# Optimization experiments

Hardware: AMD Instinct MI355X
Metric: run time of the kernel (lower is better)

The kernel has to match this reference:

```python
import jax, jax.numpy as jnp
import numpy as np

N_T = 100  # number of time grid points for the ODE solve, matching torch.linspace(0, 1, 100)


def setup_inputs() -> dict:
    key = jax.random.key(0)
    kx, kw, kb, kc, kd = jax.random.split(key, 5)
    H = 1024
    N = 16384
    return {
        "x": jax.random.normal(kx, (N, H), dtype=jnp.float32),
        "W": jax.random.normal(kw, (H, H), dtype=jnp.float32),
        "b": jax.random.normal(kb, (H,), dtype=jnp.float32),
        "c": jax.random.normal(kc, (H,), dtype=jnp.float32),
        "d": jax.random.normal(kd, (H,), dtype=jnp.float32),
    }


def reference(x, W, b, c, d):
    # fused matmul + trig elementwise: z = x @ W + b*sin(x) + c*cos(x) + d*tan(x)
    z = jnp.matmul(x, W) + b * jnp.sin(x) + c * jnp.cos(x) + d * jnp.tan(x)

    # ODE: dy/dt = -y + t*z, y(0)=0, integrated on linspace(0,1,100), return y(1).
    ts = jnp.linspace(0.0, 1.0, N_T, dtype=z.dtype)
    t0 = ts[:-1]
    dts = ts[1:] - ts[:-1]

    def f(t, y):
        return -y + t * z

    def rk4_step(y, t_dt):
        t, dt = t_dt
        k1 = f(t, y)
        k2 = f(t + 0.5 * dt, y + 0.5 * dt * k1)
        k3 = f(t + 0.5 * dt, y + 0.5 * dt * k2)
        k4 = f(t + dt, y + dt * k3)
        y_next = y + (dt / 6.0) * (k1 + 2.0 * k2 + 2.0 * k3 + k4)
        return y_next, None

    y0 = jnp.zeros_like(z)
    y_final, _ = jax.lax.scan(rk4_step, y0, (t0, dts))
    return y_final
```

## Files before the change

### kernel.cpp

```cpp
#include <hip/hip_runtime.h>
#include <hip/hip_bf16.h>

typedef __attribute__((ext_vector_type(4))) float  f32x4;
typedef __attribute__((ext_vector_type(8))) short  bf16x8;
typedef __attribute__((ext_vector_type(4))) short  bf16x4v;

#define EPAD 68
#define AS1 __attribute__((address_space(1)))
#define AS3 __attribute__((address_space(3)))

__device__ __forceinline__ unsigned short f2bf(float f) {
  __hip_bfloat16 h = __float2bfloat16(f);
  unsigned short u; __builtin_memcpy(&u, &h, 2); return u;
}
__device__ __forceinline__ float bf2f(short u) {
  unsigned int w = ((unsigned int)(unsigned short)u) << 16;
  float f; __builtin_memcpy(&f, &w, 4); return f;
}

__device__ __forceinline__ void my_sincos(float xf, float& s_out, float& c_out) {
  const float kf = __builtin_rintf(xf * 0.636619772367581343f);
  const int   q  = (int)kf;
  const double kd = (double)kf;
  double rd = __builtin_fma(-kd, 1.5707963267948966,    (double)xf);
  rd        = __builtin_fma(-kd, 6.123233995736766e-17, rd);
  const float r = (float)rd;
  const float z = r * r;
  const float ps = fmaf(z, fmaf(z, fmaf(z, 2.7183114939898219e-06f,
                                           -1.9839334836096632e-04f),
                                   8.3333293858894632e-03f),
                        -1.6666666641626524e-01f);
  const float sr = fmaf(r * z, ps, r);
  const float pc = fmaf(z, fmaf(z, fmaf(z, 2.4390448796277409e-05f,
                                           -1.3886763774609929e-03f),
                                   4.1666623323739063e-02f),
                        -4.9999999725103100e-01f);
  const float cr = fmaf(z, pc, 1.0f);
  const bool swap = (q & 1) != 0;
  float s1 = swap ? cr : sr;
  float c1 = swap ? sr : cr;
  if (q & 2)       s1 = -s1;
  if ((q + 1) & 2) c1 = -c1;
  s_out = s1; c_out = c1;
}

__global__ __launch_bounds__(256)
void prep_all(const float* __restrict__ W, const float* __restrict__ x,
              const float* __restrict__ bv, const float* __restrict__ cv,
              const float* __restrict__ dv,
              unsigned short* __restrict__ Wt, unsigned short* __restrict__ xb,
              unsigned short* __restrict__ g, int H, int n4) {
  __shared__ float tile[64][65];
  const int t = threadIdx.x;
  if (blockIdx.x < 256) {
    const int blk = blockIdx.x;
    const int n0 = (blk & 15) << 6;
    const int k0 = (blk >> 4) << 6;
    #pragma unroll
    for (int it = 0; it < 4; ++it) {
      int q = it * 256 + t;
      int r = q >> 4, c4 = (q & 15) << 2;
      f32x4 v = *(const f32x4*)&W[(size_t)(k0 + r) * H + n0 + c4];
      tile[r][c4 + 0] = v[0]; tile[r][c4 + 1] = v[1];
      tile[r][c4 + 2] = v[2]; tile[r][c4 + 3] = v[3];
    }
    __syncthreads();
    #pragma unroll
    for (int it = 0; it < 4; ++it) {
      int q = it * 256 + t;
      int r = q >> 4, c4 = (q & 15) << 2;
      bf16x4v o;
      #pragma unroll
      for (int j = 0; j < 4; ++j) o[j] = (short)f2bf(tile[c4 + j][r]);
      *(bf16x4v*)&Wt[(size_t)(n0 + r) * H + k0 + c4] = o;
    }
  } else {
    const int jm = (H >> 2) - 1;
    int i = (blockIdx.x - 256) * 256 + t;
    const int stride = ((int)gridDim.x - 256) * 256;
    for (; i < n4; i += stride) {
      f32x4 v = ((const f32x4*)x)[i];
      const int j4 = (i & jm) << 2;
      f32x4 b4 = *(const f32x4*)&bv[j4];
      f32x4 c4 = *(const f32x4*)&cv[j4];
      f32x4 d4 = *(const f32x4*)&dv[j4];
      bf16x4v xo, go;
      #pragma unroll
      for (int e = 0; e < 4; ++e) {
        xo[e] = (short)f2bf(v[e]);
        float s, co;
        my_sincos(v[e], s, co);
        const float tn = s * __builtin_amdgcn_rcpf(co);
        go[e] = (short)f2bf(fmaf(b4[e], s, fmaf(c4[e], co, d4[e] * tn)));
      }
      ((bf16x4v*)xb)[i] = xo;
      ((bf16x4v*)g)[i]  = go;
    }
  }
}

__global__ __launch_bounds__(256)
void transpose_W(const float* __restrict__ W, unsigned short* __restrict__ Wt, int H) {
  __shared__ float tile[64][65];
  const int k0 = blockIdx.y * 64;
  const int n0 = blockIdx.x * 64;
  const int t = threadIdx.x;
  #pragma unroll
  for (int it = 0; it < 4; ++it) {
    int q = it * 256 + t;
    int r = q >> 4, c4 = (q & 15) << 2;
    f32x4 v = *(const f32x4*)&W[(size_t)(k0 + r) * H + n0 + c4];
    tile[r][c4 + 0] = v[0]; tile[r][c4 + 1] = v[1];
    tile[r][c4 + 2] = v[2]; tile[r][c4 + 3] = v[3];
  }
  __syncthreads();
  #pragma unroll
  for (int it = 0; it < 4; ++it) {
    int q = it * 256 + t;
    int r = q >> 4, c4 = (q & 15) << 2;
    bf16x4v o;
    #pragma unroll
    for (int j = 0; j < 4; ++j) o[j] = (short)f2bf(tile[c4 + j][r]);
    *(bf16x4v*)&Wt[(size_t)(n0 + r) * H + k0 + c4] = o;
  }
}
__global__ __launch_bounds__(256)
void cvt_x(const float* __restrict__ x, unsigned short* __restrict__ xb, int n4) {
  int i = blockIdx.x * 256 + threadIdx.x;
  const int stride = gridDim.x * 256;
  for (; i < n4; i += stride) {
    f32x4 v = ((const f32x4*)x)[i];
    bf16x4v o;
    #pragma unroll
    for (int j = 0; j < 4; ++j) o[j] = (short)f2bf(v[j]);
    ((bf16x4v*)xb)[i] = o;
  }
}

__global__ __launch_bounds__(512, 2)
void gemm_256(const unsigned short* __restrict__ xb,
              const unsigned short* __restrict__ Wt,
              const unsigned short* __restrict__ g,
              float* __restrict__ out, float S, int H) {
  __shared__ unsigned char smem[98304];
  float* Es = (float*)smem;

  const int tid  = threadIdx.x;
  const int nwg  = gridDim.x;
  const int work = (blockIdx.x & 7) * (nwg >> 3) + (blockIdx.x >> 3);
  const int nbj  = H >> 8;
  const int bj   = work % nbj;
  const int bi   = work / nbj;
  const int i0   = bi * 256, j0 = bj * 256;
  const int wave = tid >> 6, lane = tid & 63;
  const int wr   = wave >> 2, wc = wave & 3;
  const int l16  = lane & 15, lq = lane >> 4;

  const unsigned short *aS0, *aS1, *bS0, *bS1;
  {
    const int D0 = tid * 16,        sup0 = D0 >> 7;
    const int sl0 = ((D0 >> 4) & 7) ^ (sup0 & 7);
    const int r0  = sup0 * 2 + (sl0 >> 2), c0 = (sl0 & 3) << 3;
    const int D1 = 8192 + tid * 16, sup1 = D1 >> 7;
    const int sl1 = ((D1 >> 4) & 7) ^ (sup1 & 7);
    const int r1  = sup1 * 2 + (sl1 >> 2), c1 = (sl1 & 3) << 3;
    aS0 = &xb[(size_t)(i0 + r0) * H + c0];
    aS1 = &xb[(size_t)(i0 + r1) * H + c1];
    bS0 = &Wt[(size_t)(j0 + r0) * H + c0];
    bS1 = &Wt[(size_t)(j0 + r1) * H + c1];
  }

  #define STAGE(bufq, kOff)                                                     \
    do {                                                                        \
      char* _b = (char*)smem + (bufq) * 32768;                                  \
      __builtin_amdgcn_global_load_lds((const AS1 void*)(aS0 + (kOff)),         \
        (AS3 void*)(_b + tid * 16), 16, 0, 0);                                  \
      __builtin_amdgcn_global_load_lds((const AS1 void*)(aS1 + (kOff)),         \
        (AS3 void*)(_b + 8192 + tid * 16), 16, 0, 0);                           \
      __builtin_amdgcn_global_load_lds((const AS1 void*)(bS0 + (kOff)),         \
        (AS3 void*)(_b + 16384 + tid * 16), 16, 0, 0);                          \
      __builtin_amdgcn_global_load_lds((const AS1 void*)(bS1 + (kOff)),         \
        (AS3 void*)(_b + 24576 + tid * 16), 16, 0, 0);                          \
    } while (0)

  const int slot  = (4 * (l16 & 1) + lq) ^ ((l16 >> 1) & 7);
  const int laneT = (l16 >> 1) * 128 + slot * 16;
  const int aBase = wr * 8192 + laneT;
  const int bBase = wc * 4096 + laneT;

  f32x4 acc[8][4] = {};

  const int nsteps = H >> 5;
  STAGE(0, 0);
  STAGE(1, 32);
  int bufc = 0;
  for (int t = 0; t < nsteps; ++t) {
    if (t + 2 < nsteps) {
      int buf2 = bufc + 2; if (buf2 >= 3) buf2 -= 3;
      STAGE(buf2, (t + 2) * 32);
      asm volatile("s_waitcnt vmcnt(8)" ::: "memory");
    } else if (t + 2 == nsteps) {
      asm volatile("s_waitcnt vmcnt(4)" ::: "memory");
    } else {
      asm volatile("s_waitcnt vmcnt(0)" ::: "memory");
    }
    __builtin_amdgcn_s_barrier();
    asm volatile("" ::: "memory");
    const char* Ab = (const char*)smem + bufc * 32768;
    const char* Bb = Ab + 16384;
    bf16x8 bfr[4];
    #pragma unroll
    for (int ni = 0; ni < 4; ++ni)
      bfr[ni] = *(const bf16x8*)(Bb + bBase + ni * 1024);
    __builtin_amdgcn_s_setprio(1);
    #pragma unroll
    for (int mi = 0; mi < 8; ++mi) {
      bf16x8 af = *(const bf16x8*)(Ab + aBase + mi * 1024);
      #pragma unroll
      for (int ni = 0; ni < 4; ++ni)
        acc[mi][ni] = __builtin_amdgcn_mfma_f32_16x16x32_bf16(af, bfr[ni], acc[mi][ni], 0, 0, 0);
    }
    __builtin_amdgcn_s_setprio(0);
    asm volatile("" ::: "memory");
    __builtin_amdgcn_s_barrier();
    bufc += 1; if (bufc == 3) bufc = 0;
  }
  #undef STAGE
  __syncthreads();

  float* ep = Es + wave * (16 * EPAD);
  const int rr = lane >> 2;
  const int cq = (lane & 3) * 16;
  #pragma unroll
  for (int mi = 0; mi < 8; ++mi) {
    #pragma unroll
    for (int ni = 0; ni < 4; ++ni)
      #pragma unroll
      for (int r = 0; r < 4; ++r)
        ep[(lq * 4 + r) * EPAD + ni * 16 + l16] = acc[mi][ni][r];
    const int i  = i0 + wr * 128 + mi * 16 + rr;
    const int jb = j0 + wc * 64 + cq;
    float* orow = &out[(size_t)i * H + jb];
    const unsigned short* grow = &g[(size_t)i * H + jb];
    #pragma unroll
    for (int t = 0; t < 4; ++t) {
      f32x4 a = *(const f32x4*)&ep[rr * EPAD + cq + 4 * t];
      bf16x4v gv = *(const bf16x4v*)&grow[4 * t];
      f32x4 o;
      #pragma unroll
      for (int e = 0; e < 4; ++e) o[e] = S * (a[e] + bf2f(gv[e]));
      *(f32x4*)&orow[4 * t] = o;
    }
  }
}

template <int MODE>
__global__ __launch_bounds__(256, 2)
void gemm_fb(const float* __restrict__ x, const unsigned short* __restrict__ xb,
             const unsigned short* __restrict__ Wt,
             const float* __restrict__ bv, const float* __restrict__ cv,
             const float* __restrict__ dv, float* __restrict__ out,
             float S, int H) {
  __shared__ unsigned char smem[36864];
  unsigned short* As = (unsigned short*)smem;
  unsigned short* Bs = As + 128 * 72;
  float*          Es = (float*)smem;

  const int tid  = threadIdx.x;
  const int nwg  = gridDim.x;
  const int work = (nwg % 8 == 0) ? (blockIdx.x & 7) * (nwg >> 3) + (blockIdx.x >> 3)
                                  : blockIdx.x;
  const int nbj  = H / 128;
  const int bj   = work % nbj;
  const int bi   = work / nbj;
  const int i0   = bi * 128, j0 = bj * 128;
  const int wave = tid >> 6, lane = tid & 63;
  const int wr = wave >> 1, wc = wave & 1;
  const int l16 = lane & 15, lq = lane >> 4;

  f32x4 acc[4][4] = {};
  for (int kk = 0; kk < H; kk += 64) {
    if constexpr (MODE == 1) {
      #pragma unroll
      for (int it = 0; it < 4; ++it) {
        int q = it * 256 + tid;
        int r = q >> 3, c8 = (q & 7) << 3;
        *(bf16x8*)&As[r * 72 + c8] = *(const bf16x8*)&xb[(size_t)(i0 + r) * H + kk + c8];
      }
    } else {
      #pragma unroll
      for (int it = 0; it < 8; ++it) {
        int q = it * 256 + tid;
        int r = q >> 4, c4 = (q & 15) << 2;
        f32x4 v = *(const f32x4*)&x[(size_t)(i0 + r) * H + kk + c4];
        bf16x4v o;
        #pragma unroll
        for (int j = 0; j < 4; ++j) o[j] = (short)f2bf(v[j]);
        *(bf16x4v*)&As[r * 72 + c4] = o;
      }
    }
    #pragma unroll
    for (int it = 0; it < 4; ++it) {
      int q = it * 256 + tid;
      int r = q >> 3, c8 = (q & 7) << 3;
      *(bf16x8*)&Bs[r * 72 + c8] = *(const bf16x8*)&Wt[(size_t)(j0 + r) * H + kk + c8];
    }
    __syncthreads();
    #pragma unroll
    for (int s = 0; s < 2; ++s) {
      bf16x8 af[4], bfr[4];
      #pragma unroll
      for (int mi = 0; mi < 4; ++mi)
        af[mi] = *(const bf16x8*)&As[(wr * 64 + mi * 16 + l16) * 72 + s * 32 + lq * 8];
      #pragma unroll
      for (int ni = 0; ni < 4; ++ni)
        bfr[ni] = *(const bf16x8*)&Bs[(wc * 64 + ni * 16 + l16) * 72 + s * 32 + lq * 8];
      #pragma unroll
      for (int mi = 0; mi < 4; ++mi)
        #pragma unroll
        for (int ni = 0; ni < 4; ++ni)
          acc[mi][ni] = __builtin_amdgcn_mfma_f32_16x16x32_bf16(af[mi], bfr[ni], acc[mi][ni], 0, 0, 0);
    }
    __syncthreads();
  }
  float* ep = Es + wave * (16 * EPAD);
  const int rr = lane >> 2;
  const int cq = (lane & 3) * 16;
  #pragma unroll
  for (int mi = 0; mi < 4; ++mi) {
    #pragma unroll
    for (int ni = 0; ni < 4; ++ni)
      #pragma unroll
      for (int r = 0; r < 4; ++r)
        ep[(lq * 4 + r) * EPAD + ni * 16 + l16] = acc[mi][ni][r];
    const int i  = i0 + wr * 64 + mi * 16 + rr;
    const int jb = j0 + wc * 64 + cq;
    const float* xrow = &x[(size_t)i * H + jb];
    float*       orow = &out[(size_t)i * H + jb];
    #pragma unroll
    for (int t = 0; t < 4; ++t) {
      f32x4 a  = *(const f32x4*)&ep[rr * EPAD + cq + 4 * t];
      f32x4 xv = *(const f32x4*)&xrow[4 * t];
      f32x4 b4 = *(const f32x4*)&bv[jb + 4 * t];
      f32x4 c4 = *(const f32x4*)&cv[jb + 4 * t];
      f32x4 d4 = *(const f32x4*)&dv[jb + 4 * t];
      f32x4 o;
      #pragma unroll
      for (int e = 0; e < 4; ++e) {
        float s, co;
        my_sincos(xv[e], s, co);
        const float tanv = s * __builtin_amdgcn_rcpf(co);
        o[e] = S * (fmaf(b4[e], s, a[e]) + fmaf(c4[e], co, d4[e] * tanv));
      }
      *(f32x4*)&orow[4 * t] = o;
    }
  }
}

extern "C" void kernel_launch(void* const* d_in, const int* in_sizes, int n_in,
                              void* d_out, int out_size, void* d_ws, size_t ws_size,
                              hipStream_t stream) {
  const float* x = (const float*)d_in[0];
  const float* W = (const float*)d_in[1];
  const float* b = (const float*)d_in[2];
  const float* c = (const float*)d_in[3];
  const float* d = (const float*)d_in[4];
  float* out = (float*)d_out;
  const int H = in_sizes[2];
  const int M = in_sizes[0] / H;

  const int NT = 100;
  float ts[NT];
  const float step = (float)(1.0 / 99.0);
  for (int i = 0; i < NT; ++i) ts[i] = (float)i * step;
  ts[NT - 1] = 1.0f;
  double yy = 0.0;
  for (int i = 0; i < NT - 1; ++i) {
    const double t = (double)ts[i], dt = (double)(ts[i + 1] - ts[i]);
    const double k1 = t - yy;
    const double k2 = (t + 0.5 * dt) - (yy + 0.5 * dt * k1);
    const double k3 = (t + 0.5 * dt) - (yy + 0.5 * dt * k2);
    const double k4 = (t + dt) - (yy + dt * k3);
    yy += dt / 6.0 * (k1 + 2.0 * k2 + 2.0 * k3 + k4);
  }
  const float S = (float)yy;

  unsigned short* Wt = (unsigned short*)d_ws;
  unsigned short* xb = Wt + (size_t)H * H;
  unsigned short* g  = xb + (size_t)M * H;
  const size_t needW  = (size_t)H * H * 2;
  const size_t needXb = (size_t)M * H * 2;
  const int n4 = M * H / 4;

  const int nblk256 = (M / 256) * (H / 256);
  const bool shapeOK = (H % 256 == 0) && (M % 256 == 0) && (nblk256 % 8 == 0)
                    && ((H >> 5) >= 3);

  if (ws_size >= needW + 2 * needXb && shapeOK) {
    prep_all<<<256 + 2048, 256, 0, stream>>>(W, x, b, c, d, Wt, xb, g, H, n4);
    gemm_256<<<nblk256, 512, 0, stream>>>(xb, Wt, g, out, S, H);
  } else if (ws_size >= needW + needXb) {
    dim3 tgrid(H / 64, H / 64);
    transpose_W<<<tgrid, 256, 0, stream>>>(W, Wt, H);
    cvt_x<<<2048, 256, 0, stream>>>(x, xb, n4);
    gemm_fb<1><<<(H / 128) * (M / 128), 256, 0, stream>>>(x, xb, Wt, b, c, d, out, S, H);
  } else {
    dim3 tgrid(H / 64, H / 64);
    transpose_W<<<tgrid, 256, 0, stream>>>(W, Wt, H);
    gemm_fb<2><<<(H / 128) * (M / 128), 256, 0, stream>>>(x, nullptr, Wt, b, c, d, out, S, H);
  }
}
```

Baseline: 81.30 us.

## Split GEMM main loop into two MFMA phases interleaved with staged loads

Restructures the triple-buffered bf16 GEMM loop so each K-step runs two half-phases. Each phase preloads its LDS fragments, issues half of the next global-to-LDS stage (A first, then B), and only then runs its MFMA cluster. The aim is to spread global loads and LDS reads across the compute phases instead of issuing all staging at the loop top. The cost is extra barriers per iteration and more delicate vmcnt accounting across the split stages.

```diff
diff --git a/kernel.cpp b/kernel.cpp
--- a/kernel.cpp
+++ b/kernel.cpp
@@ -170,62 +170,89 @@
     bS1 = &Wt[(size_t)(j0 + r1) * H + c1];
   }
 
-  #define STAGE(bufq, kOff)                                                     \
+  #define STAGE_A(sl, kOff)                                                     \
     do {                                                                        \
-      char* _b = (char*)smem + (bufq) * 32768;                                  \
+      char* _b = (char*)smem + (sl) * 32768;                                    \
       __builtin_amdgcn_global_load_lds((const AS1 void*)(aS0 + (kOff)),         \
         (AS3 void*)(_b + tid * 16), 16, 0, 0);                                  \
       __builtin_amdgcn_global_load_lds((const AS1 void*)(aS1 + (kOff)),         \
         (AS3 void*)(_b + 8192 + tid * 16), 16, 0, 0);                           \
+    } while (0)
+  #define STAGE_B(sl, kOff)                                                     \
+    do {                                                                        \
+      char* _b = (char*)smem + (sl) * 32768;                                    \
       __builtin_amdgcn_global_load_lds((const AS1 void*)(bS0 + (kOff)),         \
         (AS3 void*)(_b + 16384 + tid * 16), 16, 0, 0);                          \
       __builtin_amdgcn_global_load_lds((const AS1 void*)(bS1 + (kOff)),         \
         (AS3 void*)(_b + 24576 + tid * 16), 16, 0, 0);                          \
     } while (0)
 
-  const int slot  = (4 * (l16 & 1) + lq) ^ ((l16 >> 1) & 7);
-  const int laneT = (l16 >> 1) * 128 + slot * 16;
+  const int slotx = (4 * (l16 & 1) + lq) ^ ((l16 >> 1) & 7);
+  const int laneT = (l16 >> 1) * 128 + slotx * 16;
   const int aBase = wr * 8192 + laneT;
   const int bBase = wc * 4096 + laneT;
 
   f32x4 acc[8][4] = {};
 
-  const int nsteps = H >> 5;
-  STAGE(0, 0);
-  STAGE(1, 32);
-  int bufc = 0;
-  for (int t = 0; t < nsteps; ++t) {
-    if (t + 2 < nsteps) {
-      int buf2 = bufc + 2; if (buf2 >= 3) buf2 -= 3;
-      STAGE(buf2, (t + 2) * 32);
-      asm volatile("s_waitcnt vmcnt(8)" ::: "memory");
-    } else if (t + 2 == nsteps) {
+  const int nt = H >> 5;
+  STAGE_A(0, 0);  STAGE_B(0, 0);
+  STAGE_A(1, 32); STAGE_B(1, 32);
+  asm volatile("s_waitcnt vmcnt(4)" ::: "memory");
+  __builtin_amdgcn_s_barrier();
+
+  int slot = 0;
+  for (int t = 0; t < nt; ++t) {
+    const char* Ab = (const char*)smem + slot * 32768;
+    const char* Bb = Ab + 16384;
+    int s2 = slot + 2; if (s2 >= 3) s2 -= 3;
+    const int k2 = (t + 2) * 32;
+    const bool more = (t + 2) < nt;
+
+    bf16x8 afA[4], bfr[4];
+    #pragma unroll
+    for (int mi = 0; mi < 4; ++mi) afA[mi] = *(const bf16x8*)(Ab + aBase + mi * 1024);
+    #pragma unroll
+    for (int ni = 0; ni < 4; ++ni) bfr[ni] = *(const bf16x8*)(Bb + bBase + ni * 1024);
+    asm volatile("" ::: "memory");
+    if (more) STAGE_A(s2, k2);
+    __builtin_amdgcn_s_barrier();
+    asm volatile("s_waitcnt lgkmcnt(0)" ::: "memory");
+    __builtin_amdgcn_sched_barrier(0);
+    __builtin_amdgcn_s_setprio(1);
+    #pragma unroll
+    for (int mi = 0; mi < 4; ++mi)
+      #pragma unroll
+      for (int ni = 0; ni < 4; ++ni)
+        acc[mi][ni] = __builtin_amdgcn_mfma_f32_16x16x32_bf16(afA[mi], bfr[ni], acc[mi][ni], 0, 0, 0);
+    __builtin_amdgcn_s_setprio(0);
+    __builtin_amdgcn_s_barrier();
+
+    bf16x8 afB[4];
+    #pragma unroll
+    for (int mi = 0; mi < 4; ++mi) afB[mi] = *(const bf16x8*)(Ab + aBase + (mi + 4) * 1024);
+    asm volatile("" ::: "memory");
+    if (more) {
+      STAGE_B(s2, k2);
       asm volatile("s_waitcnt vmcnt(4)" ::: "memory");
-    } else {
+    } else if (t + 1 < nt) {
       asm volatile("s_waitcnt vmcnt(0)" ::: "memory");
     }
     __builtin_amdgcn_s_barrier();
-    asm volatile("" ::: "memory");
-    const char* Ab = (const char*)smem + bufc * 32768;
-    const char* Bb = Ab + 16384;
-    bf16x8 bfr[4];
-    #pragma unroll
-    for (int ni = 0; ni < 4; ++ni)
-      bfr[ni] = *(const bf16x8*)(Bb + bBase + ni * 1024);
+    asm volatile("s_waitcnt lgkmcnt(0)" ::: "memory");
+    __builtin_amdgcn_sched_barrier(0);
     __builtin_amdgcn_s_setprio(1);
     #pragma unroll
-    for (int mi = 0; mi < 8; ++mi) {
-      bf16x8 af = *(const bf16x8*)(Ab + aBase + mi * 1024);
+    for (int mi = 0; mi < 4; ++mi)
       #pragma unroll
       for (int ni = 0; ni < 4; ++ni)
-        acc[mi][ni] = __builtin_amdgcn_mfma_f32_16x16x32_bf16(af, bfr[ni], acc[mi][ni], 0, 0, 0);
-    }
+        acc[mi + 4][ni] = __builtin_amdgcn_mfma_f32_16x16x32_bf16(afB[mi], bfr[ni], acc[mi + 4][ni], 0, 0, 0);
     __builtin_amdgcn_s_setprio(0);
-    asm volatile("" ::: "memory");
     __builtin_amdgcn_s_barrier();
-    bufc += 1; if (bufc == 3) bufc = 0;
-  }
-  #undef STAGE
+
+    slot += 1; if (slot == 3) slot = 0;
+  }
+  #undef STAGE_A
+  #undef STAGE_B
   __syncthreads();
 
   float* ep = Es + wave * (16 * EPAD);
```

New measurement: 81.35 us. About the same (+0.1%).
